# Optimization experiments

Measured on AMD Instinct MI355X. Metric: run time of the kernel, lower is better.

## Reference

```python
import jax, jax.numpy as jnp
import numpy as np

ENC = 768
DEC = 768
B, T, S = 16, 1024, 1024


def setup_inputs() -> dict:
    key = jax.random.key(0)
    k1, k2, k3 = jax.random.split(key, 3)
    inputs = jax.random.normal(k1, (B, T, DEC), dtype=jnp.float32)
    context = jax.random.normal(k2, (B, S, ENC), dtype=jnp.float32)
    # linear_out: Linear(dec+enc -> dec) with bias; torch weight layout [out, in]
    W_out = jax.random.normal(k3, (DEC, DEC + ENC), dtype=jnp.float32) * 0.02
    b_out = jnp.zeros((DEC,), dtype=jnp.float32)
    w_scale = jnp.ones((1, 1, 1), dtype=jnp.float32)   # self.weight
    b_scale = jnp.ones((1, 1, 1), dtype=jnp.float32)   # self.bias
    prelu_a = jnp.full((1,), 0.25, dtype=jnp.float32)  # PReLU single param
    return {"inputs": inputs, "context": context, "W_out": W_out,
            "b_out": b_out, "w_scale": w_scale, "b_scale": b_scale,
            "prelu_a": prelu_a}


def reference(inputs, context, W_out, b_out, w_scale, b_scale, prelu_a):
    # score: bmm(h_t, h_s^T). NOTE: linear_in output is discarded in the
    # original (h_t reassigned), so the raw inputs are used — faithful here.
    align = jnp.einsum('btd,bsd->bts', inputs, context)        # [B,T,S]
    av = jax.nn.softmax(align, axis=-1)                        # softmax over src
    # gate: sigmoid of per-source column-sum over target positions
    gate = jax.nn.sigmoid(jnp.sum(av, axis=1, keepdims=True))  # [B,1,S]
    # AdaptiveAvgPool1d(1): mean over last (src) dim -> [B,T,1]
    pooled = jnp.mean(av, axis=-1, keepdims=True)
    av_g = av * gate * pooled                                  # fused elementwise
    c = jnp.einsum('bts,bsd->btd', av_g, context)              # [B,T,ENC]
    c = c * w_scale + b_scale                                  # scalar affine
    concat_c = jnp.concatenate([c, inputs], axis=-1)           # [B,T,ENC+DEC]
    h = jnp.einsum('btk,dk->btd', concat_c, W_out) + b_out     # linear_out
    attn_h = jnp.where(h >= 0, h, prelu_a * h)                 # PReLU
    return attn_h.transpose(1, 0, 2), av_g.transpose(1, 0, 2)
```

## Files before the change

kernel.cpp:

```cpp
#include <hip/hip_runtime.h>

#define B_ 16
#define T_ 1024
#define S_ 1024
#define D_ 768
#define K3_ 1536
#define BS_ (B_ * S_)
#define BD_ (B_ * D_)
#define NI_ (B_ * T_ * D_)
#define NW_ (D_ * K3_)

typedef __attribute__((ext_vector_type(8))) _Float16 half8;
typedef __attribute__((ext_vector_type(4))) float float4v;

__device__ __forceinline__ unsigned short f2h(float x) {
    return __builtin_bit_cast(unsigned short, (_Float16)x);
}
__device__ __forceinline__ float h2f(unsigned short u) {
    return (float)__builtin_bit_cast(_Float16, u);
}
__device__ __forceinline__ unsigned pkh2(float a, float b) {
    return (unsigned)f2h(a) | ((unsigned)f2h(b) << 16);
}
__device__ __forceinline__ uint2 pkh4(const float4 v) {
    return make_uint2(pkh2(v.x, v.y), pkh2(v.z, v.w));
}

__device__ __forceinline__ void gl_lds16(const void* g, void* l) {
    __builtin_amdgcn_global_load_lds(
        (const __attribute__((address_space(1))) unsigned int*)g,
        (__attribute__((address_space(3))) unsigned int*)l,
        16, 0, 0);
}

#define MFMA_PROLOG() \
    const int tid  = threadIdx.x; \
    const int w    = tid >> 6; \
    const int wm   = (w >> 1) * 64; \
    const int wn   = (w & 1) * 64; \
    const int lane = tid & 63; \
    const int q    = lane >> 4; \
    const int lr   = lane & 15; \
    float4v acc[4][4] = {};

#define STAGE_PROLOG() \
    const int rl0 = (w << 5) + (lane >> 2); \
    const int cc  = ((lane & 3) ^ ((lane >> 3) & 3)) * 8; \
    const int wb  = w * 1024; \
    const int qa  = (q ^ ((lr >> 1) & 3)) * 8;

#define MFMA_COMPUTE_F16(AP, BP) \
    { \
        half8 afr[4], bfr[4]; \
        _Pragma("unroll") \
        for (int i = 0; i < 4; i++) \
            afr[i] = *(const half8*)&(AP)[(wm + i * 16 + lr) * 32 + qa]; \
        _Pragma("unroll") \
        for (int j = 0; j < 4; j++) \
            bfr[j] = *(const half8*)&(BP)[(wn + j * 16 + lr) * 32 + qa]; \
        _Pragma("unroll") \
        for (int i = 0; i < 4; i++) \
            _Pragma("unroll") \
            for (int j = 0; j < 4; j++) \
                acc[i][j] = __builtin_amdgcn_mfma_f32_16x16x32_f16( \
                    afr[i], bfr[j], acc[i][j], 0, 0, 0); \
    }

__global__ __launch_bounds__(256) void prep_all(
    const float* __restrict__ ctx, const float* __restrict__ inp,
    const float* __restrict__ W,
    unsigned short* __restrict__ ctxT, unsigned short* __restrict__ ctx_h,
    unsigned short* __restrict__ inp_h, unsigned short* __restrict__ W_h)
{
    __shared__ unsigned short Ts[64 * 68];
    const int bid = blockIdx.x;
    const int tid = threadIdx.x;
    if (bid < 3072) {
        const int b   = bid / 192;
        const int rem = bid - b * 192;
        const int d0  = (rem >> 4) * 64;
        const int s0  = (rem & 15) * 64;
        const int srel = tid >> 4;
        const int dcol = (tid & 15) * 4;
#pragma unroll
        for (int r = 0; r < 4; r++) {
            const int s = srel + r * 16;
            float4 v = *(const float4*)(ctx + ((size_t)b * S_ + s0 + s) * D_ + d0 + dcol);
            Ts[(dcol + 0) * 68 + s] = f2h(v.x);
            Ts[(dcol + 1) * 68 + s] = f2h(v.y);
            Ts[(dcol + 2) * 68 + s] = f2h(v.z);
            Ts[(dcol + 3) * 68 + s] = f2h(v.w);
            *(uint2*)(ctx_h + ((size_t)b * S_ + s0 + s) * D_ + d0 + dcol) = pkh4(v);
        }
        __syncthreads();
        const int drow = tid >> 2;
        const int scg  = (tid & 3) * 16;
        unsigned short* dst = ctxT + ((size_t)b * D_ + d0 + drow) * S_ + s0 + scg;
#pragma unroll
        for (int p = 0; p < 4; p++) {
            uint2 u = *(const uint2*)&Ts[drow * 68 + scg + p * 4];
            *(uint2*)(dst + p * 4) = u;
        }
    } else {
        const size_t i4 = (size_t)(bid - 3072) * 256 + tid;
        const size_t flat = i4 * 4;
        float4 v;
        unsigned short* dst;
        if (flat < NI_) {
            v = ((const float4*)inp)[i4];
            dst = inp_h + flat;
        } else {
            v = *(const float4*)(W + (flat - NI_));
            dst = W_h + (flat - NI_);
        }
        *(uint2*)dst = pkh4(v);
    }
}

__global__ __launch_bounds__(256) void gemm_scores_f16(
    const unsigned short* __restrict__ ctx_h,
    const unsigned short* __restrict__ inp_h,
    unsigned short* __restrict__ sc_h)
{
    const int hwid = blockIdx.x + (blockIdx.y << 3) + (blockIdx.z << 6);
    const int wk   = (hwid & 7) * 128 + (hwid >> 3);
    const int b  = wk >> 6;
    const int t0 = ((wk >> 3) & 7) * 128;
    const int s0 = (wk & 7) * 128;

    __shared__ __align__(16) unsigned short As[2 * 128 * 32];
    __shared__ __align__(16) unsigned short Bs[2 * 128 * 32];

    MFMA_PROLOG();
    STAGE_PROLOG();

    const unsigned short* ga0 = ctx_h + ((size_t)b * S_ + s0 + rl0) * D_ + cc;
    const unsigned short* ga1 = ga0 + (size_t)16 * D_;
    const unsigned short* gb0 = inp_h + ((size_t)b * T_ + t0 + rl0) * D_ + cc;
    const unsigned short* gb1 = gb0 + (size_t)16 * D_;

#define STAGE_G1(bi, kb) \
    { \
        gl_lds16(ga0 + (kb), &As[(bi) * 4096 + wb]); \
        gl_lds16(ga1 + (kb), &As[(bi) * 4096 + wb + 512]); \
        gl_lds16(gb0 + (kb), &Bs[(bi) * 4096 + wb]); \
        gl_lds16(gb1 + (kb), &Bs[(bi) * 4096 + wb + 512]); \
    }

    STAGE_G1(0, 0);
    __syncthreads();
    int cur = 0;
    for (int kb = 32; kb < D_; kb += 32) {
        const int nxt = cur ^ 1;
        STAGE_G1(nxt, kb);
        MFMA_COMPUTE_F16(&As[cur * 4096], &Bs[cur * 4096]);
        __syncthreads();
        cur = nxt;
    }
    MFMA_COMPUTE_F16(&As[cur * 4096], &Bs[cur * 4096]);

#pragma unroll
    for (int i = 0; i < 4; i++)
#pragma unroll
        for (int j = 0; j < 4; j++) {
            const int t = t0 + wn + j * 16 + lr;
            const int s = s0 + wm + i * 16 + q * 4;
            uint2 o;
            o.x = pkh2(acc[i][j][0], acc[i][j][1]);
            o.y = pkh2(acc[i][j][2], acc[i][j][3]);
            *(uint2*)(sc_h + (size_t)t * BS_ + (size_t)b * S_ + s) = o;
        }
}

__global__ __launch_bounds__(256) void softmax_rows(
    unsigned short* __restrict__ sc)
{
    const int bid = blockIdx.x;
    const int b = bid & (B_ - 1);
    const int t = bid / B_;
    unsigned short* row = sc + (size_t)t * BS_ + (size_t)b * S_;
    const int tid = threadIdx.x;

    uint2 u = *(const uint2*)(row + tid * 4);
    float v0 = h2f((unsigned short)(u.x & 0xffff)), v1 = h2f((unsigned short)(u.x >> 16));
    float v2 = h2f((unsigned short)(u.y & 0xffff)), v3 = h2f((unsigned short)(u.y >> 16));
    float m = fmaxf(fmaxf(v0, v1), fmaxf(v2, v3));
#pragma unroll
    for (int off = 32; off > 0; off >>= 1) m = fmaxf(m, __shfl_xor(m, off));

    __shared__ float red[8];
    if ((tid & 63) == 0) red[tid >> 6] = m;
    __syncthreads();
    m = fmaxf(fmaxf(red[0], red[1]), fmaxf(red[2], red[3]));

    float e0 = __expf(v0 - m), e1 = __expf(v1 - m);
    float e2 = __expf(v2 - m), e3 = __expf(v3 - m);
    float s = (e0 + e1) + (e2 + e3);
#pragma unroll
    for (int off = 32; off > 0; off >>= 1) s += __shfl_xor(s, off);
    if ((tid & 63) == 0) red[4 + (tid >> 6)] = s;
    __syncthreads();
    s = (red[4] + red[5]) + (red[6] + red[7]);

    const float inv = 1.0f / s;
    uint2 o;
    o.x = pkh2(e0 * inv, e1 * inv);
    o.y = pkh2(e2 * inv, e3 * inv);
    *(uint2*)(row + tid * 4) = o;
}

__global__ __launch_bounds__(256) void colsum_part(
    const unsigned short* __restrict__ av_h, float* __restrict__ partial)
{
    const int b = blockIdx.y;
    const int c = blockIdx.z;
    const int s2 = blockIdx.x * 512 + threadIdx.x * 2;
    const unsigned short* p = av_h + (size_t)(c * 128) * BS_ + (size_t)b * S_ + s2;
    float s0 = 0.0f, s1 = 0.0f;
#pragma unroll 8
    for (int t = 0; t < 128; t++) {
        const unsigned u = *(const unsigned*)(p + (size_t)t * BS_);
        s0 += h2f((unsigned short)(u & 0xffff));
        s1 += h2f((unsigned short)(u >> 16));
    }
    *(float2*)(partial + ((size_t)c * B_ + b) * S_ + s2) = make_float2(s0, s1);
}

__global__ __launch_bounds__(256) void gate_final(
    const float* __restrict__ partial, float* __restrict__ gate)
{
    const int idx = blockIdx.x * 256 + threadIdx.x;
    const int b = idx >> 10, s = idx & (S_ - 1);
    float sum = 0.0f;
#pragma unroll
    for (int c = 0; c < T_ / 128; c++) sum += partial[((size_t)c * B_ + b) * S_ + s];
    gate[idx] = 1.0f / (1.0f + __expf(-sum));
}

__global__ __launch_bounds__(256) void av_out(
    unsigned short* __restrict__ av_h, const float* __restrict__ gate,
    float* __restrict__ out2)
{
    const size_t i8 = ((size_t)blockIdx.x * 256 + threadIdx.x) * 8;
    const int s = (int)(i8 & (S_ - 1));
    const int b = (int)((i8 >> 10) & (B_ - 1));
    const uint4 u = *(const uint4*)(av_h + i8);
    const float4 g0 = *(const float4*)(gate + b * S_ + s);
    const float4 g1 = *(const float4*)(gate + b * S_ + s + 4);
    float a0 = h2f((unsigned short)(u.x & 0xffff)) * g0.x, a1 = h2f((unsigned short)(u.x >> 16)) * g0.y;
    float a2 = h2f((unsigned short)(u.y & 0xffff)) * g0.z, a3 = h2f((unsigned short)(u.y >> 16)) * g0.w;
    float a4 = h2f((unsigned short)(u.z & 0xffff)) * g1.x, a5 = h2f((unsigned short)(u.z >> 16)) * g1.y;
    float a6 = h2f((unsigned short)(u.w & 0xffff)) * g1.z, a7 = h2f((unsigned short)(u.w >> 16)) * g1.w;
    const float is = 1.0f / (float)S_;
    *(float4*)(out2 + i8)     = make_float4(a0 * is, a1 * is, a2 * is, a3 * is);
    *(float4*)(out2 + i8 + 4) = make_float4(a4 * is, a5 * is, a6 * is, a7 * is);
    uint4 o;
    o.x = pkh2(a0, a1); o.y = pkh2(a2, a3);
    o.z = pkh2(a4, a5); o.w = pkh2(a6, a7);
    *(uint4*)(av_h + i8) = o;
}

__global__ __launch_bounds__(256) void gemm_ctx_f16(
    const unsigned short* __restrict__ ctxT, const unsigned short* __restrict__ av_h,
    const float* __restrict__ w_scale, const float* __restrict__ b_scale,
    unsigned short* __restrict__ c_h)
{
    const int hwid = blockIdx.x + blockIdx.y * 8 + blockIdx.z * 48;
    const int wk   = (hwid & 7) * 96 + (hwid >> 3);
    const int t0 = (wk % 8) * 128;
    const int d0 = ((wk / 8) % 6) * 128;
    const int b  = wk / 48;

    __shared__ __align__(16) unsigned short As[2 * 128 * 32];
    __shared__ __align__(16) unsigned short Bs[2 * 128 * 32];

    MFMA_PROLOG();
    STAGE_PROLOG();

    const unsigned short* ga0 = ctxT + ((size_t)b * D_ + d0 + rl0) * S_ + cc;
    const unsigned short* ga1 = ga0 + (size_t)16 * S_;
    const unsigned short* gb0 = av_h + (size_t)(t0 + rl0) * BS_ + (size_t)b * S_ + cc;
    const unsigned short* gb1 = gb0 + (size_t)16 * BS_;

#define STAGE_G2(bi, sbk) \
    { \
        gl_lds16(ga0 + (sbk), &As[(bi) * 4096 + wb]); \
        gl_lds16(ga1 + (sbk), &As[(bi) * 4096 + wb + 512]); \
        gl_lds16(gb0 + (sbk), &Bs[(bi) * 4096 + wb]); \
        gl_lds16(gb1 + (sbk), &Bs[(bi) * 4096 + wb + 512]); \
    }

    STAGE_G2(0, 0);
    __syncthreads();
    int cur = 0;
    for (int sb = 32; sb < S_; sb += 32) {
        const int nxt = cur ^ 1;
        STAGE_G2(nxt, sb);
        MFMA_COMPUTE_F16(&As[cur * 4096], &Bs[cur * 4096]);
        __syncthreads();
        cur = nxt;
    }
    MFMA_COMPUTE_F16(&As[cur * 4096], &Bs[cur * 4096]);

    const float wsc = w_scale[0] * (1.0f / (float)S_);
    const float bsc = b_scale[0];
#pragma unroll
    for (int i = 0; i < 4; i++)
#pragma unroll
        for (int j = 0; j < 4; j++) {
            const int d = d0 + wm + i * 16 + q * 4;
            const int t = t0 + wn + j * 16 + lr;
            uint2 o;
            o.x = pkh2(acc[i][j][0] * wsc + bsc, acc[i][j][1] * wsc + bsc);
            o.y = pkh2(acc[i][j][2] * wsc + bsc, acc[i][j][3] * wsc + bsc);
            *(uint2*)(c_h + ((size_t)b * T_ + t) * D_ + d) = o;
        }
}

__global__ __launch_bounds__(256) void gemm_out_f16(
    const unsigned short* __restrict__ c_h, const unsigned short* __restrict__ inp_h,
    const unsigned short* __restrict__ W_h, const float* __restrict__ bias,
    const float* __restrict__ prelu_a, float* __restrict__ out0)
{
    const int hwid = blockIdx.x + blockIdx.y * 6;
    const int wk   = (hwid & 7) * 96 + (hwid >> 3);
    const int d0 = (wk % 6) * 128;
    const int n0 = (wk / 6) * 128;

    __shared__ __align__(16) unsigned short As[2 * 128 * 32];
    __shared__ __align__(16) unsigned short Bs[2 * 128 * 32];

    MFMA_PROLOG();
    STAGE_PROLOG();

    const unsigned short* ga0  = W_h + (size_t)(d0 + rl0) * K3_ + cc;
    const unsigned short* ga1  = ga0 + (size_t)16 * K3_;
    const unsigned short* gbc0 = c_h + (size_t)(n0 + rl0) * D_ + cc;
    const unsigned short* gbi0 = inp_h + (size_t)(n0 + rl0) * D_ + cc;

#define STAGE_G3(bi, kb) \
    { \
        const unsigned short* gbx = ((kb) < D_) ? gbc0 + (kb) : gbi0 + ((kb) - D_); \
        gl_lds16(ga0 + (kb), &As[(bi) * 4096 + wb]); \
        gl_lds16(ga1 + (kb), &As[(bi) * 4096 + wb + 512]); \
        gl_lds16(gbx, &Bs[(bi) * 4096 + wb]); \
        gl_lds16(gbx + (size_t)16 * D_, &Bs[(bi) * 4096 + wb + 512]); \
    }

    STAGE_G3(0, 0);
    __syncthreads();
    int cur = 0;
    for (int kb = 32; kb < K3_; kb += 32) {
        const int nxt = cur ^ 1;
        STAGE_G3(nxt, kb);
        MFMA_COMPUTE_F16(&As[cur * 4096], &Bs[cur * 4096]);
        __syncthreads();
        cur = nxt;
    }
    MFMA_COMPUTE_F16(&As[cur * 4096], &Bs[cur * 4096]);

    const float pa = prelu_a[0];
#pragma unroll
    for (int i = 0; i < 4; i++) {
        const int d = d0 + wm + i * 16 + q * 4;
        const float4 bz = *(const float4*)(bias + d);
#pragma unroll
        for (int j = 0; j < 4; j++) {
            const int n = n0 + wn + j * 16 + lr;
            const int bb = n >> 10;
            const int t = n & (T_ - 1);
            float4 h;
            h.x = acc[i][j][0] + bz.x;
            h.y = acc[i][j][1] + bz.y;
            h.z = acc[i][j][2] + bz.z;
            h.w = acc[i][j][3] + bz.w;
            h.x = h.x >= 0.0f ? h.x : pa * h.x;
            h.y = h.y >= 0.0f ? h.y : pa * h.y;
            h.z = h.z >= 0.0f ? h.z : pa * h.z;
            h.w = h.w >= 0.0f ? h.w : pa * h.w;
            *(float4*)(out0 + (size_t)t * BD_ + (size_t)bb * D_ + d) = h;
        }
    }
}

extern "C" void kernel_launch(void* const* d_in, const int* in_sizes, int n_in,
                              void* d_out, int out_size, void* d_ws, size_t ws_size,
                              hipStream_t stream)
{
    const float* inputs  = (const float*)d_in[0];
    const float* context = (const float*)d_in[1];
    const float* W_out   = (const float*)d_in[2];
    const float* b_out   = (const float*)d_in[3];
    const float* w_scale = (const float*)d_in[4];
    const float* b_scale = (const float*)d_in[5];
    const float* prelu_a = (const float*)d_in[6];

    float* out0 = (float*)d_out;
    float* out2 = out0 + (size_t)T_ * B_ * D_;

    unsigned short* c_h   = (unsigned short*)d_ws;
    unsigned short* ctxT  = c_h   + (size_t)B_ * T_ * D_;
    unsigned short* av_h  = ctxT  + (size_t)B_ * D_ * S_;
    unsigned short* inp_h = av_h  + (size_t)T_ * B_ * S_;
    unsigned short* W_h   = inp_h + (size_t)B_ * T_ * D_;
    float* gate    = (float*)(W_h + (size_t)NW_);
    float* partial = gate + (size_t)B_ * S_;

    prep_all<<<3072 + (NI_ + NW_) / 4 / 256, 256, 0, stream>>>(
        context, inputs, W_out, ctxT, c_h, inp_h, W_h);
    gemm_scores_f16<<<dim3(S_ / 128, T_ / 128, B_), 256, 0, stream>>>(
        c_h , inp_h, av_h);
    softmax_rows<<<B_ * T_, 256, 0, stream>>>(av_h);
    colsum_part<<<dim3(S_ / 512, B_, T_ / 128), 256, 0, stream>>>(av_h, partial);
    gate_final<<<(B_ * S_) / 256, 256, 0, stream>>>(partial, gate);
    av_out<<<(int)(((size_t)T_ * B_ * S_ / 8) / 256), 256, 0, stream>>>(
        av_h, gate, out2);
    gemm_ctx_f16<<<dim3(T_ / 128, D_ / 128, B_), 256, 0, stream>>>(
        ctxT, av_h, w_scale, b_scale, c_h);
    gemm_out_f16<<<dim3(D_ / 128, (B_ * T_) / 128), 256, 0, stream>>>(
        c_h, inp_h, W_h, b_out, prelu_a, out0);
}
```

Measured before the change: 396.5 us.

## Fuse softmax with column-sum via atomics and drop LDS swizzle

Replaces the separate softmax, partial column-sum and gate kernels with one kernel. Each block normalises 8 rows and atomically adds the per-column sums into a buffer that prep_all now zeroes. The sigmoid moves into av_out. This removes a full re-read of the probability matrix and two kernel launches. It also removes the XOR swizzle from the shared-memory staging and fragment reads in the MFMA GEMMs, which may bring back LDS bank conflicts, and float atomics make the column sums order-dependent.

```diff
diff --git a/kernel.cpp b/kernel.cpp
--- a/kernel.cpp
+++ b/kernel.cpp
@@ -9,6 +9,8 @@
 #define BD_ (B_ * D_)
 #define NI_ (B_ * T_ * D_)
 #define NW_ (D_ * K3_)
+#define NPRE_ 13440
+#define ZBASE_ (3072 + NPRE_)
 
 typedef __attribute__((ext_vector_type(8))) _Float16 half8;
 typedef __attribute__((ext_vector_type(4))) float float4v;
@@ -45,19 +47,18 @@
 
 #define STAGE_PROLOG() \
     const int rl0 = (w << 5) + (lane >> 2); \
-    const int cc  = ((lane & 3) ^ ((lane >> 3) & 3)) * 8; \
-    const int wb  = w * 1024; \
-    const int qa  = (q ^ ((lr >> 1) & 3)) * 8;
+    const int cc  = (lane & 3) * 8; \
+    const int wb  = w * 1024;
 
 #define MFMA_COMPUTE_F16(AP, BP) \
     { \
         half8 afr[4], bfr[4]; \
         _Pragma("unroll") \
         for (int i = 0; i < 4; i++) \
-            afr[i] = *(const half8*)&(AP)[(wm + i * 16 + lr) * 32 + qa]; \
+            afr[i] = *(const half8*)&(AP)[(wm + i * 16 + lr) * 32 + q * 8]; \
         _Pragma("unroll") \
         for (int j = 0; j < 4; j++) \
-            bfr[j] = *(const half8*)&(BP)[(wn + j * 16 + lr) * 32 + qa]; \
+            bfr[j] = *(const half8*)&(BP)[(wn + j * 16 + lr) * 32 + q * 8]; \
         _Pragma("unroll") \
         for (int i = 0; i < 4; i++) \
             _Pragma("unroll") \
@@ -70,7 +71,8 @@
     const float* __restrict__ ctx, const float* __restrict__ inp,
     const float* __restrict__ W,
     unsigned short* __restrict__ ctxT, unsigned short* __restrict__ ctx_h,
-    unsigned short* __restrict__ inp_h, unsigned short* __restrict__ W_h)
+    unsigned short* __restrict__ inp_h, unsigned short* __restrict__ W_h,
+    float* __restrict__ colsum)
 {
     __shared__ unsigned short Ts[64 * 68];
     const int bid = blockIdx.x;
@@ -101,7 +103,7 @@
             uint2 u = *(const uint2*)&Ts[drow * 68 + scg + p * 4];
             *(uint2*)(dst + p * 4) = u;
         }
-    } else {
+    } else if (bid < ZBASE_) {
         const size_t i4 = (size_t)(bid - 3072) * 256 + tid;
         const size_t flat = i4 * 4;
         float4 v;
@@ -114,6 +116,9 @@
             dst = W_h + (flat - NI_);
         }
         *(uint2*)dst = pkh4(v);
+    } else {
+        const int i4 = (bid - ZBASE_) * 256 + tid;
+        *(float4*)(colsum + (size_t)i4 * 4) = make_float4(0.f, 0.f, 0.f, 0.f);
     }
 }
 
@@ -172,85 +177,81 @@
         }
 }
 
-__global__ __launch_bounds__(256) void softmax_rows(
-    unsigned short* __restrict__ sc)
-{
-    const int bid = blockIdx.x;
-    const int b = bid & (B_ - 1);
-    const int t = bid / B_;
-    unsigned short* row = sc + (size_t)t * BS_ + (size_t)b * S_;
+__global__ __launch_bounds__(256) void softmax_colsum(
+    unsigned short* __restrict__ sc, float* __restrict__ colsum)
+{
+    const int b  = blockIdx.x;
+    const int t0 = blockIdx.y * 8;
     const int tid = threadIdx.x;
-
-    uint2 u = *(const uint2*)(row + tid * 4);
-    float v0 = h2f((unsigned short)(u.x & 0xffff)), v1 = h2f((unsigned short)(u.x >> 16));
-    float v2 = h2f((unsigned short)(u.y & 0xffff)), v3 = h2f((unsigned short)(u.y >> 16));
-    float m = fmaxf(fmaxf(v0, v1), fmaxf(v2, v3));
-#pragma unroll
-    for (int off = 32; off > 0; off >>= 1) m = fmaxf(m, __shfl_xor(m, off));
-
     __shared__ float red[8];
-    if ((tid & 63) == 0) red[tid >> 6] = m;
-    __syncthreads();
-    m = fmaxf(fmaxf(red[0], red[1]), fmaxf(red[2], red[3]));
-
-    float e0 = __expf(v0 - m), e1 = __expf(v1 - m);
-    float e2 = __expf(v2 - m), e3 = __expf(v3 - m);
-    float s = (e0 + e1) + (e2 + e3);
-#pragma unroll
-    for (int off = 32; off > 0; off >>= 1) s += __shfl_xor(s, off);
-    if ((tid & 63) == 0) red[4 + (tid >> 6)] = s;
-    __syncthreads();
-    s = (red[4] + red[5]) + (red[6] + red[7]);
-
-    const float inv = 1.0f / s;
-    uint2 o;
-    o.x = pkh2(e0 * inv, e1 * inv);
-    o.y = pkh2(e2 * inv, e3 * inv);
-    *(uint2*)(row + tid * 4) = o;
-}
-
-__global__ __launch_bounds__(256) void colsum_part(
-    const unsigned short* __restrict__ av_h, float* __restrict__ partial)
-{
-    const int b = blockIdx.y;
-    const int c = blockIdx.z;
-    const int s2 = blockIdx.x * 512 + threadIdx.x * 2;
-    const unsigned short* p = av_h + (size_t)(c * 128) * BS_ + (size_t)b * S_ + s2;
-    float s0 = 0.0f, s1 = 0.0f;
-#pragma unroll 8
-    for (int t = 0; t < 128; t++) {
-        const unsigned u = *(const unsigned*)(p + (size_t)t * BS_);
-        s0 += h2f((unsigned short)(u & 0xffff));
-        s1 += h2f((unsigned short)(u >> 16));
-    }
-    *(float2*)(partial + ((size_t)c * B_ + b) * S_ + s2) = make_float2(s0, s1);
-}
-
-__global__ __launch_bounds__(256) void gate_final(
-    const float* __restrict__ partial, float* __restrict__ gate)
-{
-    const int idx = blockIdx.x * 256 + threadIdx.x;
-    const int b = idx >> 10, s = idx & (S_ - 1);
-    float sum = 0.0f;
-#pragma unroll
-    for (int c = 0; c < T_ / 128; c++) sum += partial[((size_t)c * B_ + b) * S_ + s];
-    gate[idx] = 1.0f / (1.0f + __expf(-sum));
+
+    float cs0 = 0.f, cs1 = 0.f, cs2 = 0.f, cs3 = 0.f;
+    for (int r = 0; r < 8; r++) {
+        unsigned short* row = sc + (size_t)(t0 + r) * BS_ + (size_t)b * S_;
+        uint2 u = *(const uint2*)(row + tid * 4);
+        float v0 = h2f((unsigned short)(u.x & 0xffff));
+        float v1 = h2f((unsigned short)(u.x >> 16));
+        float v2 = h2f((unsigned short)(u.y & 0xffff));
+        float v3 = h2f((unsigned short)(u.y >> 16));
+
+        float m = fmaxf(fmaxf(v0, v1), fmaxf(v2, v3));
+#pragma unroll
+        for (int off = 32; off > 0; off >>= 1) m = fmaxf(m, __shfl_xor(m, off));
+        if ((tid & 63) == 0) red[tid >> 6] = m;
+        __syncthreads();
+        m = fmaxf(fmaxf(red[0], red[1]), fmaxf(red[2], red[3]));
+
+        float e0 = __expf(v0 - m), e1 = __expf(v1 - m);
+        float e2 = __expf(v2 - m), e3 = __expf(v3 - m);
+        float s = (e0 + e1) + (e2 + e3);
+#pragma unroll
+        for (int off = 32; off > 0; off >>= 1) s += __shfl_xor(s, off);
+        if ((tid & 63) == 0) red[4 + (tid >> 6)] = s;
+        __syncthreads();
+        s = (red[4] + red[5]) + (red[6] + red[7]);
+
+        const float inv = 1.0f / s;
+        e0 *= inv; e1 *= inv; e2 *= inv; e3 *= inv;
+        uint2 o;
+        o.x = pkh2(e0, e1);
+        o.y = pkh2(e2, e3);
+        *(uint2*)(row + tid * 4) = o;
+        cs0 += e0; cs1 += e1; cs2 += e2; cs3 += e3;
+        __syncthreads();
+    }
+    float* cp = colsum + (size_t)b * S_ + tid * 4;
+    atomicAdd(cp + 0, cs0);
+    atomicAdd(cp + 1, cs1);
+    atomicAdd(cp + 2, cs2);
+    atomicAdd(cp + 3, cs3);
 }
 
 __global__ __launch_bounds__(256) void av_out(
-    unsigned short* __restrict__ av_h, const float* __restrict__ gate,
+    unsigned short* __restrict__ av_h, const float* __restrict__ colsum,
     float* __restrict__ out2)
 {
     const size_t i8 = ((size_t)blockIdx.x * 256 + threadIdx.x) * 8;
     const int s = (int)(i8 & (S_ - 1));
     const int b = (int)((i8 >> 10) & (B_ - 1));
     const uint4 u = *(const uint4*)(av_h + i8);
-    const float4 g0 = *(const float4*)(gate + b * S_ + s);
-    const float4 g1 = *(const float4*)(gate + b * S_ + s + 4);
-    float a0 = h2f((unsigned short)(u.x & 0xffff)) * g0.x, a1 = h2f((unsigned short)(u.x >> 16)) * g0.y;
-    float a2 = h2f((unsigned short)(u.y & 0xffff)) * g0.z, a3 = h2f((unsigned short)(u.y >> 16)) * g0.w;
-    float a4 = h2f((unsigned short)(u.z & 0xffff)) * g1.x, a5 = h2f((unsigned short)(u.z >> 16)) * g1.y;
-    float a6 = h2f((unsigned short)(u.w & 0xffff)) * g1.z, a7 = h2f((unsigned short)(u.w >> 16)) * g1.w;
+    const float4 c0 = *(const float4*)(colsum + b * S_ + s);
+    const float4 c1 = *(const float4*)(colsum + b * S_ + s + 4);
+    const float g0 = 1.0f / (1.0f + __expf(-c0.x));
+    const float g1 = 1.0f / (1.0f + __expf(-c0.y));
+    const float g2 = 1.0f / (1.0f + __expf(-c0.z));
+    const float g3 = 1.0f / (1.0f + __expf(-c0.w));
+    const float g4 = 1.0f / (1.0f + __expf(-c1.x));
+    const float g5 = 1.0f / (1.0f + __expf(-c1.y));
+    const float g6 = 1.0f / (1.0f + __expf(-c1.z));
+    const float g7 = 1.0f / (1.0f + __expf(-c1.w));
+    float a0 = h2f((unsigned short)(u.x & 0xffff)) * g0;
+    float a1 = h2f((unsigned short)(u.x >> 16))    * g1;
+    float a2 = h2f((unsigned short)(u.y & 0xffff)) * g2;
+    float a3 = h2f((unsigned short)(u.y >> 16))    * g3;
+    float a4 = h2f((unsigned short)(u.z & 0xffff)) * g4;
+    float a5 = h2f((unsigned short)(u.z >> 16))    * g5;
+    float a6 = h2f((unsigned short)(u.w & 0xffff)) * g6;
+    float a7 = h2f((unsigned short)(u.w >> 16))    * g7;
     const float is = 1.0f / (float)S_;
     *(float4*)(out2 + i8)     = make_float4(a0 * is, a1 * is, a2 * is, a3 * is);
     *(float4*)(out2 + i8 + 4) = make_float4(a4 * is, a5 * is, a6 * is, a7 * is);
@@ -403,18 +404,15 @@
     unsigned short* av_h  = ctxT  + (size_t)B_ * D_ * S_;
     unsigned short* inp_h = av_h  + (size_t)T_ * B_ * S_;
     unsigned short* W_h   = inp_h + (size_t)B_ * T_ * D_;
-    float* gate    = (float*)(W_h + (size_t)NW_);
-    float* partial = gate + (size_t)B_ * S_;
-
-    prep_all<<<3072 + (NI_ + NW_) / 4 / 256, 256, 0, stream>>>(
-        context, inputs, W_out, ctxT, c_h, inp_h, W_h);
+    float* colsum  = (float*)(W_h + (size_t)NW_);
+
+    prep_all<<<ZBASE_ + 16, 256, 0, stream>>>(
+        context, inputs, W_out, ctxT, c_h, inp_h, W_h, colsum);
     gemm_scores_f16<<<dim3(S_ / 128, T_ / 128, B_), 256, 0, stream>>>(
         c_h , inp_h, av_h);
-    softmax_rows<<<B_ * T_, 256, 0, stream>>>(av_h);
-    colsum_part<<<dim3(S_ / 512, B_, T_ / 128), 256, 0, stream>>>(av_h, partial);
-    gate_final<<<(B_ * S_) / 256, 256, 0, stream>>>(partial, gate);
+    softmax_colsum<<<dim3(B_, T_ / 8), 256, 0, stream>>>(av_h, colsum);
     av_out<<<(int)(((size_t)T_ * B_ * S_ / 8) / 256), 256, 0, stream>>>(
-        av_h, gate, out2);
+        av_h, colsum, out2);
     gemm_ctx_f16<<<dim3(T_ / 128, D_ / 128, B_), 256, 0, stream>>>(
         ctxT, av_h, w_scale, b_scale, c_h);
     gemm_out_f16<<<dim3(D_ / 128, (B_ * T_) / 128), 256, 0, stream>>>(
```

After: 422.2 us. 1.06x slower.
